# Kernel optimization log

Measured on AMD Instinct MI355X. Metric: run time of the kernel, lower is better.

The kernel has to match this reference:

```python
import jax, jax.numpy as jnp
import numpy as np

THRESH = 0.5
DECAY = 0.2
N_NODES = 39
T = 2000
K_HOPS = 3


def setup_inputs() -> dict:
    key = jax.random.key(0)
    ks = jax.random.split(key, 10)
    x = jax.random.normal(ks[0], (N_NODES, 2, T), dtype=jnp.float32)
    edge_index = jax.random.randint(ks[1], (2, 156), 0, N_NODES)
    # TAGConv(2, 64, K=3): (K+1) bias-free hop weights + single bias
    W_conv = jax.random.normal(ks[2], (K_HOPS + 1, 2, 64), dtype=jnp.float32) * 0.3
    b_conv = jax.random.normal(ks[3], (64,), dtype=jnp.float32) * 0.05
    W1 = jax.random.normal(ks[4], (N_NODES * 64, 128), dtype=jnp.float32) * 0.02
    b1 = jax.random.normal(ks[5], (128,), dtype=jnp.float32) * 0.02
    W2 = jax.random.normal(ks[6], (128, 256), dtype=jnp.float32) * 0.08
    b2 = jax.random.normal(ks[7], (256,), dtype=jnp.float32) * 0.02
    W3 = jax.random.normal(ks[8], (256, 36), dtype=jnp.float32) * 0.06
    b3 = jax.random.normal(ks[9], (36,), dtype=jnp.float32) * 0.02
    return {"x": x, "edge_index": edge_index, "W_conv": W_conv, "b_conv": b_conv,
            "W1": W1, "b1": b1, "W2": W2, "b2": b2, "W3": W3, "b3": b3}


def _norm_adj(edge_index, dtype):
    # PyG gcn_norm without self loops: A_hat = D^-1/2 A D^-1/2, message flows row->col
    row, col = edge_index[0], edge_index[1]
    A = jnp.zeros((N_NODES, N_NODES), dtype).at[col, row].add(1.0)
    deg = A.sum(axis=1)
    dinv = jnp.where(deg > 0, deg ** -0.5, 0.0).astype(dtype)
    return dinv[:, None] * A * dinv[None, :]


def reference(x, edge_index, W_conv, b_conv, W1, b1, W2, b2, W3, b3):
    A_hat = _norm_adj(edge_index, x.dtype)

    def spike(m):
        return (m > THRESH).astype(m.dtype)

    def step(carry, xt):
        c1m, c1s, h1m, h1s, h2m, h2s, h3m, h3s, acc = carry
        # TAGConv: sum_k (A_hat^k xt) @ W_k + bias   [39,64]
        h = xt
        conv = h @ W_conv[0]
        for k in range(1, K_HOPS + 1):
            h = A_hat @ h
            conv = conv + h @ W_conv[k]
        conv = conv + b_conv
        c1m = c1m * DECAY * (1.0 - c1s) + conv
        c1s = spike(c1m)
        f = c1s.reshape(-1)  # [2496]
        h1m = h1m * DECAY * (1.0 - h1s) + f @ W1 + b1
        h1s = spike(h1m)
        h2m = h2m * DECAY * (1.0 - h2s) + h1s @ W2 + b2
        h2s = spike(h2m)
        h3m = h3m * DECAY * (1.0 - h3s) + h2s @ W3 + b3
        h3s = spike(h3m)
        return (c1m, c1s, h1m, h1s, h2m, h2s, h3m, h3s, acc + h3s), None

    z = lambda s: jnp.zeros(s, x.dtype)
    init = (z((N_NODES, 64)), z((N_NODES, 64)), z((128,)), z((128,)),
            z((256,)), z((256,)), z((36,)), z((36,)), z((36,)))
    xs = jnp.moveaxis(x, -1, 0)  # [T, 39, 2]
    carry, _ = jax.lax.scan(step, init, xs)
    return carry[-1] / x.shape[-1]
```

## Files before the change

### kernel.cpp

```cpp
#include <hip/hip_runtime.h>

#define T 2000
#define K1N 2496
#define K2 4992
#define TL 48
#define WL 16
#define NCHB 42
#define TLA 8
#define MAXNZ 24

using short8 = __attribute__((ext_vector_type(8))) short;
using floatx4 = __attribute__((ext_vector_type(4))) float;

__device__ __forceinline__ unsigned bf16_rne(float v) {
    unsigned u = __float_as_uint(v);
    return (u + 0x7FFFu + ((u >> 16) & 1u)) >> 16;
}
__device__ __forceinline__ unsigned packhl(float w) {
    unsigned hi = bf16_rne(w);
    float r = w - __uint_as_float(hi << 16);
    unsigned lo = bf16_rne(r);
    return (hi & 0xFFFFu) | (lo << 16);
}

__global__ __launch_bounds__(256) void hops(const float* __restrict__ x,
        const int* __restrict__ ei, float* __restrict__ Fg,
        const float* __restrict__ W1, unsigned* __restrict__ W1t,
        float* __restrict__ out) {
    __shared__ float ah[1560];
    __shared__ float2 alist[39 * MAXNZ];
    __shared__ int nnzr[40];
    __shared__ float bufA[78 * TLA];
    __shared__ float bufB[78 * TLA];
    __shared__ float feat[39 * TLA * 8];
    int tid = threadIdx.x;
    int bl = blockIdx.x;
    int ts = bl * TLA;

    if (bl == 0 && tid < 36) out[tid] = 0.f;

    for (int u = tid; u < 1521; u += 256) ah[u] = 0.f;
    __syncthreads();
    if (tid < 156) atomicAdd(&ah[ei[156 + tid] * 39 + ei[tid]], 1.f);
    __syncthreads();
    if (tid < 39) {
        float d = 0.f;
        for (int u = 0; u < 39; ++u) d += ah[tid * 39 + u];
        ah[1521 + tid] = (d > 0.f) ? (1.f / sqrtf(d)) : 0.f;
    }
    __syncthreads();
    for (int u = tid; u < 1521; u += 256) {
        int i = u / 39, j = u - i * 39;
        ah[u] = (ah[1521 + i] * ah[u]) * ah[1521 + j];
    }
    __syncthreads();
    if (tid < 39) {
        int cnt = 0;
        for (int m = 0; m < 39; ++m) {
            float v = ah[tid * 39 + m];
            if (v != 0.f && cnt < MAXNZ) {
                alist[tid * MAXNZ + cnt] = make_float2(v, __int_as_float((2 * m) * TLA * 4));
                ++cnt;
            }
        }
        nnzr[tid] = cnt;
    }
    __syncthreads();

    for (int e = tid; e < 78 * TLA; e += 256) {
        int r = e / TLA, tt = e - r * TLA;
        bufA[r * TLA + tt] = x[r * T + ts + tt];
    }
    __syncthreads();

    for (int e = tid; e < 78 * TLA; e += 256) {
        int r = e / TLA, tt = e - r * TLA;
        feat[((r >> 1) * TLA + tt) * 8 + (r & 1)] = bufA[r * TLA + tt];
    }
    for (int e = tid; e < 78; e += 256) {
        int r = e;
        int ii = r >> 1, c = r & 1;
        float acc[8];
        #pragma unroll
        for (int u = 0; u < 8; ++u) acc[u] = 0.f;
        int nz = nnzr[ii];
        const float2* lp = &alist[ii * MAXNZ];
        int cg = c * (TLA * 4);
        for (int q = 0; q < nz; ++q) {
            float2 av = lp[q];
            const float* xp = (const float*)((const char*)bufA + (__float_as_int(av.y) + cg));
            float a = av.x;
            float4 x0 = *(const float4*)xp;
            float4 x1 = *(const float4*)(xp + 4);
            acc[0] += a * x0.x; acc[1] += a * x0.y; acc[2] += a * x0.z; acc[3] += a * x0.w;
            acc[4] += a * x1.x; acc[5] += a * x1.y; acc[6] += a * x1.z; acc[7] += a * x1.w;
        }
        float* dp = &bufB[r * TLA];
        *(float4*)dp = *(float4*)&acc[0];
        *(float4*)(dp + 4) = *(float4*)&acc[4];
    }
    __syncthreads();

    for (int e = tid; e < 78 * TLA; e += 256) {
        int r = e / TLA, tt = e - r * TLA;
        feat[((r >> 1) * TLA + tt) * 8 + 2 + (r & 1)] = bufB[r * TLA + tt];
    }
    for (int e = tid; e < 78; e += 256) {
        int r = e;
        int ii = r >> 1, c = r & 1;
        float acc[8];
        #pragma unroll
        for (int u = 0; u < 8; ++u) acc[u] = 0.f;
        int nz = nnzr[ii];
        const float2* lp = &alist[ii * MAXNZ];
        int cg = c * (TLA * 4);
        for (int q = 0; q < nz; ++q) {
            float2 av = lp[q];
            const float* xp = (const float*)((const char*)bufB + (__float_as_int(av.y) + cg));
            float a = av.x;
            float4 x0 = *(const float4*)xp;
            float4 x1 = *(const float4*)(xp + 4);
            acc[0] += a * x0.x; acc[1] += a * x0.y; acc[2] += a * x0.z; acc[3] += a * x0.w;
            acc[4] += a * x1.x; acc[5] += a * x1.y; acc[6] += a * x1.z; acc[7] += a * x1.w;
        }
        float* dp = &bufA[r * TLA];
        *(float4*)dp = *(float4*)&acc[0];
        *(float4*)(dp + 4) = *(float4*)&acc[4];
    }
    __syncthreads();

    for (int e = tid; e < 78 * TLA; e += 256) {
        int r = e / TLA, tt = e - r * TLA;
        feat[((r >> 1) * TLA + tt) * 8 + 4 + (r & 1)] = bufA[r * TLA + tt];
    }
    for (int e = tid; e < 78; e += 256) {
        int r = e;
        int ii = r >> 1, c = r & 1;
        float acc[8];
        #pragma unroll
        for (int u = 0; u < 8; ++u) acc[u] = 0.f;
        int nz = nnzr[ii];
        const float2* lp = &alist[ii * MAXNZ];
        int cg = c * (TLA * 4);
        for (int q = 0; q < nz; ++q) {
            float2 av = lp[q];
            const float* xp = (const float*)((const char*)bufA + (__float_as_int(av.y) + cg));
            float a = av.x;
            float4 x0 = *(const float4*)xp;
            float4 x1 = *(const float4*)(xp + 4);
            acc[0] += a * x0.x; acc[1] += a * x0.y; acc[2] += a * x0.z; acc[3] += a * x0.w;
            acc[4] += a * x1.x; acc[5] += a * x1.y; acc[6] += a * x1.z; acc[7] += a * x1.w;
        }
        #pragma unroll
        for (int u = 0; u < 8; ++u)
            feat[(ii * TLA + u) * 8 + 6 + c] = acc[u];
    }
    __syncthreads();

    for (int e = tid; e < 39 * TLA * 2; e += 256) {
        int idx = e >> 1, half = e & 1;
        int n = idx / TLA, tt = idx - n * TLA;
        *(float4*)&Fg[((size_t)n * T + ts + tt) * 8 + half * 4] =
            *(const float4*)&feat[idx * 8 + half * 4];
    }

    const int total = 128 * K1N;
    for (int f = bl * 256 + tid; f < total; f += 250 * 256) {
        int k = f >> 7, jj = f & 127;
        W1t[jj * K1N + k] = packhl(W1[f]);
    }
}

__global__ __launch_bounds__(256) void scan_c1(const float* __restrict__ Fg,
        const float* __restrict__ Wc, const float* __restrict__ bc,
        unsigned char* __restrict__ FS) {
    __shared__ float featL[4 * 64 * 8];
    int tid = threadIdx.x;
    int nb = blockIdx.x, ch = blockIdx.y;
    int t0 = ch * TL;
    int hs = t0 - WL; if (hs < 0) hs = 0;
    int ncol = (t0 + TL) - hs;
    int i0 = nb * 4;

    for (int e = tid; e < 4 * ncol * 2; e += 256) {
        int idx = e >> 1, half = e & 1;
        int il = idx / ncol, cc = idx - il * ncol;
        int gn = i0 + il, t = hs + cc;
        float4 v = make_float4(0.f, 0.f, 0.f, 0.f);
        if (gn < 39 && t < T)
            v = *(const float4*)&Fg[((size_t)gn * T + t) * 8 + half * 4];
        *(float4*)&featL[(il * 64 + cc) * 8 + half * 4] = v;
    }
    __syncthreads();

    int iloc = tid >> 6, j = tid & 63;
    int n = nb * 256 + tid;
    bool vn = (i0 + iloc) < 39;
    float wv[8], bias;
    #pragma unroll
    for (int q = 0; q < 8; ++q) wv[q] = Wc[q * 64 + j];
    bias = bc[j];
    float m = 0.f, s = 0.f;

    for (int tg = 0; tg < ncol; tg += 8) {
        float4 f0a[8], f1a[8];
        #pragma unroll
        for (int u = 0; u < 8; ++u) {
            const float4* fp = (const float4*)&featL[((iloc * 64) + tg + u) * 8];
            f0a[u] = fp[0];
            f1a[u] = fp[1];
        }
        #pragma unroll
        for (int u = 0; u < 8; ++u) {
            float acc = 0.f;
            acc += wv[0] * f0a[u].x; acc += wv[1] * f0a[u].y;
            acc += wv[2] * f0a[u].z; acc += wv[3] * f0a[u].w;
            acc += wv[4] * f1a[u].x; acc += wv[5] * f1a[u].y;
            acc += wv[6] * f1a[u].z; acc += wv[7] * f1a[u].w;
            float v = acc + bias;
            m = m * 0.2f * (1.f - s) + v;
            s = (m > 0.5f) ? 1.f : 0.f;
            int t = hs + tg + u;
            if (vn && t >= t0 && t < T) FS[t * K1N + n] = (unsigned char)(s != 0.f);
        }
    }
}

__global__ __launch_bounds__(256) void gemm1(const unsigned char* __restrict__ FS,
        const short* __restrict__ W1t, float* __restrict__ F1p) {
    __shared__ short As[32 * 72];
    __shared__ short Ws[128 * 72];
    int tid = threadIdx.x;
    int t0 = blockIdx.x * 32;
    int ks = blockIdx.y;
    int lane = tid & 63, wvi = tid >> 6;
    int j0 = wvi * 32;
    int row = lane & 15, quad = lane >> 4;
    floatx4 a00 = {0.f, 0.f, 0.f, 0.f};
    floatx4 a01 = a00, a10 = a00, a11 = a00;
    int kb = ks * 416, kb2 = ks * 832;
    int sm = tid >> 3, sb4 = (tid & 7) * 4;
    int gt = t0 + sm;
    int jjv[4], kov[4];
    #pragma unroll
    for (int u = 0; u < 4; ++u) {
        int aid = u * 256 + tid;
        jjv[u] = aid >> 3;
        kov[u] = (aid & 7) * 8;
    }
    unsigned u4 = 0;
    short8 wr0, wr1, wr2, wr3;
    if (gt < T) u4 = *(const unsigned*)&FS[gt * K1N + kb + sb4];
    wr0 = *(const short8*)&W1t[jjv[0] * K2 + kb2 + kov[0]];
    wr1 = *(const short8*)&W1t[jjv[1] * K2 + kb2 + kov[1]];
    wr2 = *(const short8*)&W1t[jjv[2] * K2 + kb2 + kov[2]];
    wr3 = *(const short8*)&W1t[jjv[3] * K2 + kb2 + kov[3]];
    for (int c = 0; c < 13; ++c) {
        uint4 dd;
        dd.x = (u4 & 0x000000FFu) ? 0x3F803F80u : 0u;
        dd.y = (u4 & 0x0000FF00u) ? 0x3F803F80u : 0u;
        dd.z = (u4 & 0x00FF0000u) ? 0x3F803F80u : 0u;
        dd.w = (u4 & 0xFF000000u) ? 0x3F803F80u : 0u;
        *(uint4*)&As[sm * 72 + sb4 * 2] = dd;
        *(short8*)&Ws[jjv[0] * 72 + kov[0]] = wr0;
        *(short8*)&Ws[jjv[1] * 72 + kov[1]] = wr1;
        *(short8*)&Ws[jjv[2] * 72 + kov[2]] = wr2;
        *(short8*)&Ws[jjv[3] * 72 + kov[3]] = wr3;
        __syncthreads();
        unsigned u4n = 0;
        short8 wn0, wn1, wn2, wn3;
        if (c < 12) {
            if (gt < T) u4n = *(const unsigned*)&FS[gt * K1N + kb + (c + 1) * 32 + sb4];
            wn0 = *(const short8*)&W1t[jjv[0] * K2 + kb2 + (c + 1) * 64 + kov[0]];
            wn1 = *(const short8*)&W1t[jjv[1] * K2 + kb2 + (c + 1) * 64 + kov[1]];
            wn2 = *(const short8*)&W1t[jjv[2] * K2 + kb2 + (c + 1) * 64 + kov[2]];
            wn3 = *(const short8*)&W1t[jjv[3] * K2 + kb2 + (c + 1) * 64 + kov[3]];
        }
        #pragma unroll
        for (int sh = 0; sh < 2; ++sh) {
            int k0 = sh * 32 + quad * 8;
            short8 fa0 = *(const short8*)&As[row * 72 + k0];
            short8 fa1 = *(const short8*)&As[(row + 16) * 72 + k0];
            short8 fb0 = *(const short8*)&Ws[(j0 + row) * 72 + k0];
            short8 fb1 = *(const short8*)&Ws[(j0 + 16 + row) * 72 + k0];
            a00 = __builtin_amdgcn_mfma_f32_16x16x32_bf16(fa0, fb0, a00, 0, 0, 0);
            a01 = __builtin_amdgcn_mfma_f32_16x16x32_bf16(fa0, fb1, a01, 0, 0, 0);
            a10 = __builtin_amdgcn_mfma_f32_16x16x32_bf16(fa1, fb0, a10, 0, 0, 0);
            a11 = __builtin_amdgcn_mfma_f32_16x16x32_bf16(fa1, fb1, a11, 0, 0, 0);
        }
        __syncthreads();
        if (c < 12) { u4 = u4n; wr0 = wn0; wr1 = wn1; wr2 = wn2; wr3 = wn3; }
    }
    #pragma unroll
    for (int r = 0; r < 4; ++r) {
        int m0 = quad * 4 + r;
        int t = t0 + m0;
        if (t < T) {
            F1p[t * 768 + ks * 128 + j0 + row] = a00[r];
            F1p[t * 768 + ks * 128 + j0 + 16 + row] = a01[r];
        }
        int t2 = t0 + 16 + m0;
        if (t2 < T) {
            F1p[t2 * 768 + ks * 128 + j0 + row] = a10[r];
            F1p[t2 * 768 + ks * 128 + j0 + 16 + row] = a11[r];
        }
    }
}

__global__ __launch_bounds__(256) void h1_gemm2(const float* __restrict__ F1p,
        const float* __restrict__ b1, const float* __restrict__ W2,
        float* __restrict__ G2) {
    __shared__ float AT[128 * 8];
    int tid = threadIdx.x;
    int t0 = blockIdx.x * 8;
    if (tid < 128) {
        int n = tid;
        int hs = t0 - 16; if (hs < 0) hs = 0;
        float b = b1[n];
        float m = 0.f, s = 0.f;
        for (int tg = hs; tg < t0 + 8; tg += 4) {
            float vb[4][6];
            #pragma unroll
            for (int u = 0; u < 4; ++u)
                #pragma unroll
                for (int q = 0; q < 6; ++q)
                    vb[u][q] = F1p[(tg + u) * 768 + q * 128 + n];
            #pragma unroll
            for (int u = 0; u < 4; ++u) {
                float v = 0.f;
                #pragma unroll
                for (int q = 0; q < 6; ++q) v += vb[u][q];
                v += b;
                m = m * 0.2f * (1.f - s) + v;
                s = (m > 0.5f) ? 1.f : 0.f;
                int t = tg + u;
                if (t >= t0) AT[n * 8 + (t - t0)] = s;
            }
        }
    }
    __syncthreads();
    int j = tid;
    float acc[8] = {0.f};
    #pragma unroll 4
    for (int k = 0; k < 128; ++k) {
        float w = W2[k * 256 + j];
        float4 q0 = *(const float4*)&AT[k * 8 + 0];
        float4 q1 = *(const float4*)&AT[k * 8 + 4];
        acc[0] += q0.x * w; acc[1] += q0.y * w; acc[2] += q0.z * w; acc[3] += q0.w * w;
        acc[4] += q1.x * w; acc[5] += q1.y * w; acc[6] += q1.z * w; acc[7] += q1.w * w;
    }
    #pragma unroll
    for (int tt = 0; tt < 8; ++tt) G2[(t0 + tt) * 256 + j] = acc[tt];
}

__global__ __launch_bounds__(256) void tail(const float* __restrict__ G2,
        const float* __restrict__ b2, const float* __restrict__ W3,
        const float* __restrict__ b3, float* __restrict__ out) {
    __shared__ float w3t[36 * 260];
    __shared__ unsigned char S2[52 * 260];
    __shared__ float G3[52 * 36];
    int tid = threadIdx.x;
    int t0 = blockIdx.x * 25;
    int gs = t0 - 25; if (gs < 0) gs = 0;
    int hs = gs - 25; if (hs < 0) hs = 0;
    int L3 = t0 + 25 - gs;
    #pragma unroll
    for (int u = 0; u < 9; ++u) {
        int f = u * 1024 + tid * 4;
        float4 wq = *(const float4*)&W3[f];
        int k0 = f / 36, j0 = f - k0 * 36;
        float wv[4] = {wq.x, wq.y, wq.z, wq.w};
        #pragma unroll
        for (int q = 0; q < 4; ++q) {
            int k = (j0 + q >= 36) ? k0 + 1 : k0;
            int jj = (j0 + q >= 36) ? (j0 + q - 36) : (j0 + q);
            w3t[jj * 260 + k] = wv[q];
        }
    }
    {
        int n = tid;
        float b = b2[n];
        float m = 0.f, s = 0.f;
        for (int base = hs; base < t0 + 25; base += 25) {
            float vb[25];
            #pragma unroll
            for (int u = 0; u < 25; ++u) vb[u] = G2[(base + u) * 256 + n];
            #pragma unroll
            for (int u = 0; u < 25; ++u) {
                float v = vb[u] + b;
                m = m * 0.2f * (1.f - s) + v;
                s = (m > 0.5f) ? 1.f : 0.f;
                int t = base + u;
                if (t >= gs) S2[(t - gs) * 260 + n] = (unsigned char)(s != 0.f);
            }
        }
    }
    __syncthreads();
    for (int e = tid; e < 36 * 13; e += 256) {
        int jj = e / 13, g = e - (e / 13) * 13;
        int tb = g * 4;
        if (tb >= L3) continue;
        float ac0 = 0.f, ac1 = 0.f, ac2 = 0.f, ac3 = 0.f;
        const unsigned char* r0 = &S2[tb * 260];
        for (int k = 0; k < 256; k += 4) {
            float4 w = *(const float4*)&w3t[jj * 260 + k];
            uchar4 q0 = *(const uchar4*)&r0[k];
            uchar4 q1 = *(const uchar4*)&r0[260 + k];
            uchar4 q2 = *(const uchar4*)&r0[520 + k];
            uchar4 q3 = *(const uchar4*)&r0[780 + k];
            ac0 += (float)q0.x * w.x + (float)q0.y * w.y + (float)q0.z * w.z + (float)q0.w * w.w;
            ac1 += (float)q1.x * w.x + (float)q1.y * w.y + (float)q1.z * w.z + (float)q1.w * w.w;
            ac2 += (float)q2.x * w.x + (float)q2.y * w.y + (float)q2.z * w.z + (float)q2.w * w.w;
            ac3 += (float)q3.x * w.x + (float)q3.y * w.y + (float)q3.z * w.z + (float)q3.w * w.w;
        }
        G3[tb * 36 + jj] = ac0;
        if (tb + 1 < L3) G3[(tb + 1) * 36 + jj] = ac1;
        if (tb + 2 < L3) G3[(tb + 2) * 36 + jj] = ac2;
        if (tb + 3 < L3) G3[(tb + 3) * 36 + jj] = ac3;
    }
    __syncthreads();
    if (tid < 36) {
        int n = tid;
        float b = b3[n];
        float m = 0.f, s = 0.f;
        int cnt = 0;
        for (int t = gs; t < t0 + 25; ++t) {
            float v = G3[(t - gs) * 36 + n] + b;
            m = m * 0.2f * (1.f - s) + v;
            s = (m > 0.5f) ? 1.f : 0.f;
            if (t >= t0) cnt += (s != 0.f) ? 1 : 0;
        }
        atomicAdd(&out[n], (float)cnt * 0.0005f);
    }
}

extern "C" void kernel_launch(void* const* d_in, const int* in_sizes, int n_in,
                              void* d_out, int out_size, void* d_ws, size_t ws_size,
                              hipStream_t stream) {
    const float* x  = (const float*)d_in[0];
    const int*   ei = (const int*)d_in[1];
    const float* Wc = (const float*)d_in[2];
    const float* bc = (const float*)d_in[3];
    const float* W1 = (const float*)d_in[4];
    const float* b1 = (const float*)d_in[5];
    const float* W2 = (const float*)d_in[6];
    const float* b2 = (const float*)d_in[7];
    const float* W3 = (const float*)d_in[8];
    const float* b3 = (const float*)d_in[9];
    float* out = (float*)d_out;

    float* w = (float*)d_ws;
    float* F1p = w;                       w += (size_t)T * 768;
    float* G2  = w;                       w += (size_t)T * 256;
    float* Fg  = w;                       w += (size_t)39 * T * 8;
    unsigned* W1t = (unsigned*)w;         w += 128 * K1N;
    unsigned char* FS = (unsigned char*)w;

    hops<<<250, 256, 0, stream>>>(x, ei, Fg, W1, W1t, out);
    scan_c1<<<dim3(10, NCHB), 256, 0, stream>>>(Fg, Wc, bc, FS);
    gemm1<<<dim3(63, 6), 256, 0, stream>>>(FS, (const short*)W1t, F1p);
    h1_gemm2<<<250, 256, 0, stream>>>(F1p, b1, W2, G2);
    tail<<<80, 256, 0, stream>>>(G2, b2, W3, b3, out);
}
```

Measured before the change: 138.3 us.

## Fuse five pipeline kernels into one cooperative kernel with grid syncs

```diff
diff --git a/kernel.cpp b/kernel.cpp
--- a/kernel.cpp
+++ b/kernel.cpp
@@ -1,13 +1,21 @@
 #include <hip/hip_runtime.h>
+#include <hip/hip_cooperative_groups.h>
+
+namespace cg = cooperative_groups;
 
 #define T 2000
 #define K1N 2496
 #define K2 4992
-#define TL 48
-#define WL 16
-#define NCHB 42
 #define TLA 8
+#define TLB 80
+#define WLB 16
 #define MAXNZ 24
+#define NBLK 250
+#define SMEM_A 28864
+#define SMEM_B 12288
+#define SMEM_C 23040
+#define SMEM_D 4096
+#define SMEM_E 58448
 
 using short8 = __attribute__((ext_vector_type(8))) short;
 using floatx4 = __attribute__((ext_vector_type(4))) float;
@@ -23,18 +31,16 @@
     return (hi & 0xFFFFu) | (lo << 16);
 }
 
-__global__ __launch_bounds__(256) void hops(const float* __restrict__ x,
-        const int* __restrict__ ei, float* __restrict__ Fg,
-        const float* __restrict__ W1, unsigned* __restrict__ W1t,
-        float* __restrict__ out) {
-    __shared__ float ah[1560];
-    __shared__ float2 alist[39 * MAXNZ];
-    __shared__ int nnzr[40];
-    __shared__ float bufA[78 * TLA];
-    __shared__ float bufB[78 * TLA];
-    __shared__ float feat[39 * TLA * 8];
-    int tid = threadIdx.x;
-    int bl = blockIdx.x;
+__device__ __forceinline__ void phaseA(char* smem, int tid, int bl,
+        const float* __restrict__ x, const int* __restrict__ ei,
+        float* __restrict__ Fg, const float* __restrict__ W1,
+        unsigned* __restrict__ W1t, float* __restrict__ out) {
+    float*  ah    = (float*)smem;
+    float2* alist = (float2*)(smem + 6240);
+    int*    nnzr  = (int*)(smem + 13728);
+    float*  bufA  = (float*)(smem + 13888);
+    float*  bufB  = (float*)(smem + 16384);
+    float*  feat  = (float*)(smem + 18880);
     int ts = bl * TLA;
 
     if (bl == 0 && tid < 36) out[tid] = 0.f;
@@ -78,8 +84,7 @@
         feat[((r >> 1) * TLA + tt) * 8 + (r & 1)] = bufA[r * TLA + tt];
     }
     for (int e = tid; e < 78; e += 256) {
-        int r = e;
-        int ii = r >> 1, c = r & 1;
+        int r = e, ii = r >> 1, c = r & 1;
         float acc[8];
         #pragma unroll
         for (int u = 0; u < 8; ++u) acc[u] = 0.f;
@@ -106,8 +111,7 @@
         feat[((r >> 1) * TLA + tt) * 8 + 2 + (r & 1)] = bufB[r * TLA + tt];
     }
     for (int e = tid; e < 78; e += 256) {
-        int r = e;
-        int ii = r >> 1, c = r & 1;
+        int r = e, ii = r >> 1, c = r & 1;
         float acc[8];
         #pragma unroll
         for (int u = 0; u < 8; ++u) acc[u] = 0.f;
@@ -134,8 +138,7 @@
         feat[((r >> 1) * TLA + tt) * 8 + 4 + (r & 1)] = bufA[r * TLA + tt];
     }
     for (int e = tid; e < 78; e += 256) {
-        int r = e;
-        int ii = r >> 1, c = r & 1;
+        int r = e, ii = r >> 1, c = r & 1;
         float acc[8];
         #pragma unroll
         for (int u = 0; u < 8; ++u) acc[u] = 0.f;
@@ -165,21 +168,20 @@
     }
 
     const int total = 128 * K1N;
-    for (int f = bl * 256 + tid; f < total; f += 250 * 256) {
+    for (int f = bl * 256 + tid; f < total; f += NBLK * 256) {
         int k = f >> 7, jj = f & 127;
         W1t[jj * K1N + k] = packhl(W1[f]);
     }
 }
 
-__global__ __launch_bounds__(256) void scan_c1(const float* __restrict__ Fg,
-        const float* __restrict__ Wc, const float* __restrict__ bc,
-        unsigned char* __restrict__ FS) {
-    __shared__ float featL[4 * 64 * 8];
-    int tid = threadIdx.x;
-    int nb = blockIdx.x, ch = blockIdx.y;
-    int t0 = ch * TL;
-    int hs = t0 - WL; if (hs < 0) hs = 0;
-    int ncol = (t0 + TL) - hs;
+__device__ __forceinline__ void phaseB(char* smem, int tid, int bl,
+        const float* __restrict__ Fg, const float* __restrict__ Wc,
+        const float* __restrict__ bc, unsigned char* __restrict__ FS) {
+    float* featL = (float*)smem;
+    int nb = bl % 10, ch = bl / 10;
+    int t0 = ch * TLB;
+    int hs = t0 - WLB; if (hs < 0) hs = 0;
+    int ncol = (t0 + TLB) - hs;
     int i0 = nb * 4;
 
     for (int e = tid; e < 4 * ncol * 2; e += 256) {
@@ -189,7 +191,7 @@
         float4 v = make_float4(0.f, 0.f, 0.f, 0.f);
         if (gn < 39 && t < T)
             v = *(const float4*)&Fg[((size_t)gn * T + t) * 8 + half * 4];
-        *(float4*)&featL[(il * 64 + cc) * 8 + half * 4] = v;
+        *(float4*)&featL[(il * 96 + cc) * 8 + half * 4] = v;
     }
     __syncthreads();
 
@@ -206,7 +208,7 @@
         float4 f0a[8], f1a[8];
         #pragma unroll
         for (int u = 0; u < 8; ++u) {
-            const float4* fp = (const float4*)&featL[((iloc * 64) + tg + u) * 8];
+            const float4* fp = (const float4*)&featL[((iloc * 96) + tg + u) * 8];
             f0a[u] = fp[0];
             f1a[u] = fp[1];
         }
@@ -224,15 +226,14 @@
             if (vn && t >= t0 && t < T) FS[t * K1N + n] = (unsigned char)(s != 0.f);
         }
     }
-}
-
-__global__ __launch_bounds__(256) void gemm1(const unsigned char* __restrict__ FS,
-        const short* __restrict__ W1t, float* __restrict__ F1p) {
-    __shared__ short As[32 * 72];
-    __shared__ short Ws[128 * 72];
-    int tid = threadIdx.x;
-    int t0 = blockIdx.x * 32;
-    int ks = blockIdx.y;
+    __syncthreads();
+}
+
+__device__ __forceinline__ void phaseC_tile(char* smem, int tid, int t0, int ks,
+        const unsigned char* __restrict__ FS, const short* __restrict__ W1t,
+        float* __restrict__ F1p) {
+    short* As = (short*)smem;
+    short* Ws = (short*)(smem + 4608);
     int lane = tid & 63, wvi = tid >> 6;
     int j0 = wvi * 32;
     int row = lane & 15, quad = lane >> 4;
@@ -307,12 +308,10 @@
     }
 }
 
-__global__ __launch_bounds__(256) void h1_gemm2(const float* __restrict__ F1p,
-        const float* __restrict__ b1, const float* __restrict__ W2,
-        float* __restrict__ G2) {
-    __shared__ float AT[128 * 8];
-    int tid = threadIdx.x;
-    int t0 = blockIdx.x * 8;
+__device__ __forceinline__ void phaseD(char* smem, int tid, int t0,
+        const float* __restrict__ F1p, const float* __restrict__ b1,
+        const float* __restrict__ W2, float* __restrict__ G2) {
+    float* AT = (float*)smem;
     if (tid < 128) {
         int n = tid;
         int hs = t0 - 16; if (hs < 0) hs = 0;
@@ -351,16 +350,16 @@
     }
     #pragma unroll
     for (int tt = 0; tt < 8; ++tt) G2[(t0 + tt) * 256 + j] = acc[tt];
-}
-
-__global__ __launch_bounds__(256) void tail(const float* __restrict__ G2,
-        const float* __restrict__ b2, const float* __restrict__ W3,
-        const float* __restrict__ b3, float* __restrict__ out) {
-    __shared__ float w3t[36 * 260];
-    __shared__ unsigned char S2[52 * 260];
-    __shared__ float G3[52 * 36];
-    int tid = threadIdx.x;
-    int t0 = blockIdx.x * 25;
+    __syncthreads();
+}
+
+__device__ __forceinline__ void phaseE_tile(char* smem, int tid, int t0,
+        const float* __restrict__ G2, const float* __restrict__ b2,
+        const float* __restrict__ W3, const float* __restrict__ b3,
+        float* __restrict__ out) {
+    float* w3t = (float*)smem;
+    unsigned char* S2 = (unsigned char*)(smem + 37440);
+    float* G3 = (float*)(smem + 50960);
     int gs = t0 - 25; if (gs < 0) gs = 0;
     int hs = gs - 25; if (hs < 0) hs = 0;
     int L3 = t0 + 25 - gs;
@@ -434,6 +433,67 @@
     }
 }
 
+__global__ __launch_bounds__(256) void fused(const float* __restrict__ x,
+        const int* __restrict__ ei, const float* __restrict__ Wc,
+        const float* __restrict__ bc, const float* __restrict__ W1,
+        const float* __restrict__ b1, const float* __restrict__ W2,
+        const float* __restrict__ b2, const float* __restrict__ W3,
+        const float* __restrict__ b3, float* __restrict__ out,
+        float* __restrict__ Fg, unsigned* __restrict__ W1t,
+        unsigned char* __restrict__ FS, float* __restrict__ F1p,
+        float* __restrict__ G2) {
+    __shared__ __align__(16) char smem[SMEM_E];
+    cg::grid_group grid = cg::this_grid();
+    int tid = threadIdx.x, bl = blockIdx.x;
+
+    phaseA(smem, tid, bl, x, ei, Fg, W1, W1t, out);
+    __threadfence();
+    grid.sync();
+    phaseB(smem, tid, bl, Fg, Wc, bc, FS);
+    __threadfence();
+    grid.sync();
+    for (int bv = bl; bv < 378; bv += NBLK)
+        phaseC_tile(smem, tid, (bv / 6) * 32, bv % 6, FS, (const short*)W1t, F1p);
+    __threadfence();
+    grid.sync();
+    phaseD(smem, tid, bl * 8, F1p, b1, W2, G2);
+    __threadfence();
+    grid.sync();
+    if (bl < 80)
+        phaseE_tile(smem, tid, bl * 25, G2, b2, W3, b3, out);
+}
+
+__global__ __launch_bounds__(256) void kA(const float* __restrict__ x,
+        const int* __restrict__ ei, float* __restrict__ Fg,
+        const float* __restrict__ W1, unsigned* __restrict__ W1t,
+        float* __restrict__ out) {
+    __shared__ __align__(16) char smem[SMEM_A];
+    phaseA(smem, threadIdx.x, blockIdx.x, x, ei, Fg, W1, W1t, out);
+}
+__global__ __launch_bounds__(256) void kB(const float* __restrict__ Fg,
+        const float* __restrict__ Wc, const float* __restrict__ bc,
+        unsigned char* __restrict__ FS) {
+    __shared__ __align__(16) char smem[SMEM_B];
+    phaseB(smem, threadIdx.x, blockIdx.x, Fg, Wc, bc, FS);
+}
+__global__ __launch_bounds__(256) void kC(const unsigned char* __restrict__ FS,
+        const short* __restrict__ W1t, float* __restrict__ F1p) {
+    __shared__ __align__(16) char smem[SMEM_C];
+    phaseC_tile(smem, threadIdx.x, (blockIdx.x / 6) * 32, blockIdx.x % 6, FS, W1t, F1p);
+}
+__global__ __launch_bounds__(256) void kD(const float* __restrict__ F1p,
+        const float* __restrict__ b1, const float* __restrict__ W2,
+        float* __restrict__ G2) {
+    __shared__ __align__(16) char smem[SMEM_D];
+    phaseD(smem, threadIdx.x, blockIdx.x * 8, F1p, b1, W2, G2);
+}
+__global__ __launch_bounds__(256) void kE(const float* __restrict__ G2,
+        const float* __restrict__ b2, const float* __restrict__ W3,
+        const float* __restrict__ b3, float* __restrict__ out) {
+    __shared__ __align__(16) char smem[SMEM_E];
+    phaseE_tile(smem, threadIdx.x, blockIdx.x * 25, G2, b2, W3, b3, out);
+}
+
 extern "C" void kernel_launch(void* const* d_in, const int* in_sizes, int n_in,
                               void* d_out, int out_size, void* d_ws, size_t ws_size,
                               hipStream_t stream) {
@@ -456,9 +516,17 @@
     unsigned* W1t = (unsigned*)w;         w += 128 * K1N;
     unsigned char* FS = (unsigned char*)w;
 
-    hops<<<250, 256, 0, stream>>>(x, ei, Fg, W1, W1t, out);
-    scan_c1<<<dim3(10, NCHB), 256, 0, stream>>>(Fg, Wc, bc, FS);
-    gemm1<<<dim3(63, 6), 256, 0, stream>>>(FS, (const short*)W1t, F1p);
-    h1_gemm2<<<250, 256, 0, stream>>>(F1p, b1, W2, G2);
-    tail<<<80, 256, 0, stream>>>(G2, b2, W3, b3, out);
-}
+    void* args[] = { (void*)&x, (void*)&ei, (void*)&Wc, (void*)&bc, (void*)&W1,
+                     (void*)&b1, (void*)&W2, (void*)&b2, (void*)&W3, (void*)&b3,
+                     (void*)&out, (void*)&Fg, (void*)&W1t, (void*)&FS, (void*)&F1p,
+                     (void*)&G2 };
+    hipError_t err = hipLaunchCooperativeKernel((const void*)fused, dim3(NBLK),
+                                                dim3(256), args, 0, stream);
+    if (err != hipSuccess) {
+        kA<<<NBLK, 256, 0, stream>>>(x, ei, Fg, W1, W1t, out);
+        kB<<<NBLK, 256, 0, stream>>>(Fg, Wc, bc, FS);
+        kC<<<378, 256, 0, stream>>>(FS, (const short*)W1t, F1p);
+        kD<<<NBLK, 256, 0, stream>>>(F1p, b1, W2, G2);
+        kE<<<80, 256, 0, stream>>>(G2, b2, W3, b3, out);
+    }
+}
```

After: 368.0 us. 166% more time.

## Fuse conv spike scan into gemm1 with shared-memory spike tiles

Applied to the files above, without the earlier changes.

```diff
diff --git a/kernel.cpp b/kernel.cpp
--- a/kernel.cpp
+++ b/kernel.cpp
@@ -3,11 +3,9 @@
 #define T 2000
 #define K1N 2496
 #define K2 4992
-#define TL 48
-#define WL 16
-#define NCHB 42
 #define TLA 8
 #define MAXNZ 24
+#define NBLK 250
 
 using short8 = __attribute__((ext_vector_type(8))) short;
 using floatx4 = __attribute__((ext_vector_type(4))) float;
@@ -78,8 +76,7 @@
         feat[((r >> 1) * TLA + tt) * 8 + (r & 1)] = bufA[r * TLA + tt];
     }
     for (int e = tid; e < 78; e += 256) {
-        int r = e;
-        int ii = r >> 1, c = r & 1;
+        int r = e, ii = r >> 1, c = r & 1;
         float acc[8];
         #pragma unroll
         for (int u = 0; u < 8; ++u) acc[u] = 0.f;
@@ -106,8 +103,7 @@
         feat[((r >> 1) * TLA + tt) * 8 + 2 + (r & 1)] = bufB[r * TLA + tt];
     }
     for (int e = tid; e < 78; e += 256) {
-        int r = e;
-        int ii = r >> 1, c = r & 1;
+        int r = e, ii = r >> 1, c = r & 1;
         float acc[8];
         #pragma unroll
         for (int u = 0; u < 8; ++u) acc[u] = 0.f;
@@ -134,8 +130,7 @@
         feat[((r >> 1) * TLA + tt) * 8 + 4 + (r & 1)] = bufA[r * TLA + tt];
     }
     for (int e = tid; e < 78; e += 256) {
-        int r = e;
-        int ii = r >> 1, c = r & 1;
+        int r = e, ii = r >> 1, c = r & 1;
         float acc[8];
         #pragma unroll
         for (int u = 0; u < 8; ++u) acc[u] = 0.f;
@@ -165,82 +160,31 @@
     }
 
     const int total = 128 * K1N;
-    for (int f = bl * 256 + tid; f < total; f += 250 * 256) {
+    for (int f = bl * 256 + tid; f < total; f += NBLK * 256) {
         int k = f >> 7, jj = f & 127;
         W1t[jj * K1N + k] = packhl(W1[f]);
     }
 }
 
-__global__ __launch_bounds__(256) void scan_c1(const float* __restrict__ Fg,
-        const float* __restrict__ Wc, const float* __restrict__ bc,
-        unsigned char* __restrict__ FS) {
-    __shared__ float featL[4 * 64 * 8];
+__global__ __launch_bounds__(256) void scan_gemm1(
+        const float* __restrict__ Fg, const float* __restrict__ Wc,
+        const float* __restrict__ bc, const short* __restrict__ W1t,
+        float* __restrict__ F1p) {
+    __shared__ __align__(16) char smem[13312 + 23040];
+    unsigned char* S2 = (unsigned char*)smem;
+    float* FgL = (float*)(smem + 13312);
+    short* As  = (short*)(smem + 13312);
+    short* Ws  = (short*)(smem + 13312 + 4608);
+
     int tid = threadIdx.x;
-    int nb = blockIdx.x, ch = blockIdx.y;
-    int t0 = ch * TL;
-    int hs = t0 - WL; if (hs < 0) hs = 0;
-    int ncol = (t0 + TL) - hs;
-    int i0 = nb * 4;
-
-    for (int e = tid; e < 4 * ncol * 2; e += 256) {
-        int idx = e >> 1, half = e & 1;
-        int il = idx / ncol, cc = idx - il * ncol;
-        int gn = i0 + il, t = hs + cc;
-        float4 v = make_float4(0.f, 0.f, 0.f, 0.f);
-        if (gn < 39 && t < T)
-            v = *(const float4*)&Fg[((size_t)gn * T + t) * 8 + half * 4];
-        *(float4*)&featL[(il * 64 + cc) * 8 + half * 4] = v;
-    }
-    __syncthreads();
-
-    int iloc = tid >> 6, j = tid & 63;
-    int n = nb * 256 + tid;
-    bool vn = (i0 + iloc) < 39;
-    float wv[8], bias;
-    #pragma unroll
-    for (int q = 0; q < 8; ++q) wv[q] = Wc[q * 64 + j];
-    bias = bc[j];
-    float m = 0.f, s = 0.f;
-
-    for (int tg = 0; tg < ncol; tg += 8) {
-        float4 f0a[8], f1a[8];
-        #pragma unroll
-        for (int u = 0; u < 8; ++u) {
-            const float4* fp = (const float4*)&featL[((iloc * 64) + tg + u) * 8];
-            f0a[u] = fp[0];
-            f1a[u] = fp[1];
-        }
-        #pragma unroll
-        for (int u = 0; u < 8; ++u) {
-            float acc = 0.f;
-            acc += wv[0] * f0a[u].x; acc += wv[1] * f0a[u].y;
-            acc += wv[2] * f0a[u].z; acc += wv[3] * f0a[u].w;
-            acc += wv[4] * f1a[u].x; acc += wv[5] * f1a[u].y;
-            acc += wv[6] * f1a[u].z; acc += wv[7] * f1a[u].w;
-            float v = acc + bias;
-            m = m * 0.2f * (1.f - s) + v;
-            s = (m > 0.5f) ? 1.f : 0.f;
-            int t = hs + tg + u;
-            if (vn && t >= t0 && t < T) FS[t * K1N + n] = (unsigned char)(s != 0.f);
-        }
-    }
-}
-
-__global__ __launch_bounds__(256) void gemm1(const unsigned char* __restrict__ FS,
-        const short* __restrict__ W1t, float* __restrict__ F1p) {
-    __shared__ short As[32 * 72];
-    __shared__ short Ws[128 * 72];
-    int tid = threadIdx.x;
-    int t0 = blockIdx.x * 32;
-    int ks = blockIdx.y;
-    int lane = tid & 63, wvi = tid >> 6;
-    int j0 = wvi * 32;
-    int row = lane & 15, quad = lane >> 4;
-    floatx4 a00 = {0.f, 0.f, 0.f, 0.f};
-    floatx4 a01 = a00, a10 = a00, a11 = a00;
-    int kb = ks * 416, kb2 = ks * 832;
-    int sm = tid >> 3, sb4 = (tid & 7) * 4;
-    int gt = t0 + sm;
+    int bx = blockIdx.x, ks = blockIdx.y;
+    int t0 = bx * 32;
+    int hs = t0 - 16; if (hs < 0) hs = 0;
+    int ncol = t0 + 32 - hs;
+    int k0g = ks * 416;
+    int nd0 = k0g >> 6;
+
+    int kb2 = ks * 832;
     int jjv[4], kov[4];
     #pragma unroll
     for (int u = 0; u < 4; ++u) {
@@ -248,14 +192,61 @@
         jjv[u] = aid >> 3;
         kov[u] = (aid & 7) * 8;
     }
-    unsigned u4 = 0;
-    short8 wr0, wr1, wr2, wr3;
-    if (gt < T) u4 = *(const unsigned*)&FS[gt * K1N + kb + sb4];
-    wr0 = *(const short8*)&W1t[jjv[0] * K2 + kb2 + kov[0]];
-    wr1 = *(const short8*)&W1t[jjv[1] * K2 + kb2 + kov[1]];
-    wr2 = *(const short8*)&W1t[jjv[2] * K2 + kb2 + kov[2]];
-    wr3 = *(const short8*)&W1t[jjv[3] * K2 + kb2 + kov[3]];
+    short8 wr0 = *(const short8*)&W1t[jjv[0] * K2 + kb2 + kov[0]];
+    short8 wr1 = *(const short8*)&W1t[jjv[1] * K2 + kb2 + kov[1]];
+    short8 wr2 = *(const short8*)&W1t[jjv[2] * K2 + kb2 + kov[2]];
+    short8 wr3 = *(const short8*)&W1t[jjv[3] * K2 + kb2 + kov[3]];
+
+    for (int e = tid; e < 7 * ncol * 2; e += 256) {
+        int idx = e >> 1, half = e & 1;
+        int nl = idx / ncol, cc = idx - nl * ncol;
+        int t = hs + cc;
+        int gn = nd0 + nl;
+        float4 v = make_float4(0.f, 0.f, 0.f, 0.f);
+        if (gn < 39 && t < T)
+            v = *(const float4*)&Fg[((size_t)gn * T + t) * 8 + half * 4];
+        *(float4*)&FgL[(nl * ncol + cc) * 8 + half * 4] = v;
+    }
+    __syncthreads();
+
+    for (int cw = 0; cw < 2; ++cw) {
+        int cn = cw * 256 + tid;
+        if (cn < 416) {
+            int gk = k0g + cn;
+            int nl = (gk >> 6) - nd0;
+            int j = gk & 63;
+            float wv[8];
+            #pragma unroll
+            for (int q = 0; q < 8; ++q) wv[q] = Wc[q * 64 + j];
+            float bias = bc[j];
+            float m = 0.f, s = 0.f;
+            const float* fb = &FgL[nl * ncol * 8];
+            for (int cc = 0; cc < ncol; ++cc) {
+                float4 a0 = *(const float4*)&fb[cc * 8];
+                float4 a1 = *(const float4*)&fb[cc * 8 + 4];
+                float acc = 0.f;
+                acc += wv[0] * a0.x; acc += wv[1] * a0.y;
+                acc += wv[2] * a0.z; acc += wv[3] * a0.w;
+                acc += wv[4] * a1.x; acc += wv[5] * a1.y;
+                acc += wv[6] * a1.z; acc += wv[7] * a1.w;
+                float v = acc + bias;
+                m = m * 0.2f * (1.f - s) + v;
+                s = (m > 0.5f) ? 1.f : 0.f;
+                int t = hs + cc;
+                if (t >= t0) S2[(t - t0) * 416 + cn] = (unsigned char)(s != 0.f);
+            }
+        }
+    }
+    __syncthreads();
+
+    int lane = tid & 63, wvi = tid >> 6;
+    int j0 = wvi * 32;
+    int row = lane & 15, quad = lane >> 4;
+    floatx4 a00 = {0.f, 0.f, 0.f, 0.f};
+    floatx4 a01 = a00, a10 = a00, a11 = a00;
+    int sm = tid >> 3, sb4 = (tid & 7) * 4;
     for (int c = 0; c < 13; ++c) {
+        unsigned u4 = *(const unsigned*)&S2[sm * 416 + c * 32 + sb4];
         uint4 dd;
         dd.x = (u4 & 0x000000FFu) ? 0x3F803F80u : 0u;
         dd.y = (u4 & 0x0000FF00u) ? 0x3F803F80u : 0u;
@@ -267,10 +258,8 @@
         *(short8*)&Ws[jjv[2] * 72 + kov[2]] = wr2;
         *(short8*)&Ws[jjv[3] * 72 + kov[3]] = wr3;
         __syncthreads();
-        unsigned u4n = 0;
         short8 wn0, wn1, wn2, wn3;
         if (c < 12) {
-            if (gt < T) u4n = *(const unsigned*)&FS[gt * K1N + kb + (c + 1) * 32 + sb4];
             wn0 = *(const short8*)&W1t[jjv[0] * K2 + kb2 + (c + 1) * 64 + kov[0]];
             wn1 = *(const short8*)&W1t[jjv[1] * K2 + kb2 + (c + 1) * 64 + kov[1]];
             wn2 = *(const short8*)&W1t[jjv[2] * K2 + kb2 + (c + 1) * 64 + kov[2]];
@@ -289,7 +278,7 @@
             a11 = __builtin_amdgcn_mfma_f32_16x16x32_bf16(fa1, fb1, a11, 0, 0, 0);
         }
         __syncthreads();
-        if (c < 12) { u4 = u4n; wr0 = wn0; wr1 = wn1; wr2 = wn2; wr3 = wn3; }
+        if (c < 12) { wr0 = wn0; wr1 = wn1; wr2 = wn2; wr3 = wn3; }
     }
     #pragma unroll
     for (int r = 0; r < 4; ++r) {
@@ -454,11 +443,9 @@
     float* G2  = w;                       w += (size_t)T * 256;
     float* Fg  = w;                       w += (size_t)39 * T * 8;
     unsigned* W1t = (unsigned*)w;         w += 128 * K1N;
-    unsigned char* FS = (unsigned char*)w;
-
-    hops<<<250, 256, 0, stream>>>(x, ei, Fg, W1, W1t, out);
-    scan_c1<<<dim3(10, NCHB), 256, 0, stream>>>(Fg, Wc, bc, FS);
-    gemm1<<<dim3(63, 6), 256, 0, stream>>>(FS, (const short*)W1t, F1p);
+
+    hops<<<NBLK, 256, 0, stream>>>(x, ei, Fg, W1, W1t, out);
+    scan_gemm1<<<dim3(63, 6), 256, 0, stream>>>(Fg, Wc, bc, (const short*)W1t, F1p);
     h1_gemm2<<<250, 256, 0, stream>>>(F1p, b1, W2, G2);
     tail<<<80, 256, 0, stream>>>(G2, b2, W3, b3, out);
 }
```

Result: no change. 137.2 us (-0.8%).
